# Kernel optimization log

Measured on AMD Instinct MI355X. Metric: run time of the kernel, lower is better.

The kernel has to match this reference:

```python
import jax, jax.numpy as jnp
import numpy as np

B, T, DEMO = 64, 4096, 8
N_MOD, N_POS = 37, 10
D_IN = N_POS + 1 + N_MOD  # 48
PHI_W, LATENT = 128, 128
PSI_W, PSI_L = 128, 128
DOT, HEADS = 64, 4
RHO_W, OUT = 128, 1
MAX_TIME = 1000.0


def _dense_init(key, fan_in, fan_out):
    lim = float(np.sqrt(6.0 / fan_in))  # he_uniform-ish
    return jax.random.uniform(key, (fan_in, fan_out), jnp.float32, -lim, lim)


def setup_inputs() -> dict:
    key = jax.random.key(0)
    ks = jax.random.split(key, 32)
    inp = {}
    inp['demo'] = jax.random.normal(ks[0], (B, DEMO), jnp.float32)
    inp['times'] = jax.random.uniform(ks[1], (B, T, 1), jnp.float32, 0.0, 100.0)
    inp['values'] = jax.random.normal(ks[2], (B, T, 1), jnp.float32)
    inp['measurements'] = jax.random.randint(ks[3], (B, T), 0, N_MOD, jnp.int32)
    # all sequences full length -> N = B*(T+1) static
    inp['segment_ids'] = jnp.repeat(jnp.arange(B, dtype=jnp.int32), T + 1)
    inp['timescales'] = jnp.asarray(MAX_TIME ** np.linspace(0.0, 1.0, N_POS // 2), jnp.float32)
    inp['demo_W1'] = _dense_init(ks[4], DEMO, PHI_W); inp['demo_b1'] = jnp.zeros((PHI_W,), jnp.float32)
    inp['demo_W2'] = _dense_init(ks[5], PHI_W, D_IN); inp['demo_b2'] = jnp.zeros((D_IN,), jnp.float32)
    dims = [D_IN, PHI_W, PHI_W, PHI_W, LATENT]
    for i in range(4):
        inp['phi_W%d' % i] = _dense_init(ks[6 + i], dims[i], dims[i + 1])
        inp['phi_b%d' % i] = jnp.zeros((dims[i + 1],), jnp.float32)
    pdims = [D_IN, PSI_W, PSI_W, PSI_L]
    for i in range(3):
        inp['psi_W%d' % i] = _dense_init(ks[10 + i], pdims[i], pdims[i + 1])
        inp['psi_b%d' % i] = jnp.zeros((pdims[i + 1],), jnp.float32)
    inp['W_k'] = _dense_init(ks[13], PSI_L + D_IN, DOT * HEADS)
    # original inits W_q to zeros (degenerate uniform attention); small random keeps test non-trivial
    inp['W_q'] = jax.random.normal(ks[14], (HEADS, DOT), jnp.float32) * 0.05
    rdims = [LATENT * HEADS, RHO_W, RHO_W, RHO_W, OUT]
    for i in range(4):
        inp['rho_W%d' % i] = _dense_init(ks[15 + i], rdims[i], rdims[i + 1])
        inp['rho_b%d' % i] = jnp.zeros((rdims[i + 1],), jnp.float32)
    return inp


def _forward(demo, times, values, timescales,
             demo_W1, demo_b1, demo_W2, demo_b2,
             phi_W0, phi_b0, phi_W1, phi_b1, phi_W2, phi_b2, phi_W3, phi_b3,
             psi_W0, psi_b0, psi_W1, psi_b1, psi_W2, psi_b2,
             W_k, W_q,
             rho_W0, rho_b0, rho_W1, rho_b1, rho_W2, rho_b2, rho_W3, rho_b3,
             measurements, segment_ids):
    relu = jax.nn.relu
    nseg = demo.shape[0]
    # positional encoding: times [B,T,1] / timescales [5] -> sin|cos -> [B,T,10]
    scaled = times / timescales[None, None, :]
    tt = jnp.concatenate([jnp.sin(scaled), jnp.cos(scaled)], axis=-1)
    meas = jax.nn.one_hot(measurements, N_MOD, dtype=times.dtype)  # [B,T,37]
    combined = jnp.concatenate([tt, values, meas], axis=-1)        # [B,T,48]
    demo_enc = relu(demo @ demo_W1 + demo_b1) @ demo_W2 + demo_b2  # [B,48]
    x = jnp.concatenate([demo_enc[:, None, :], combined], axis=1)  # [B,T+1,48]
    collected = x.reshape(-1, x.shape[-1])                         # [N,48]
    # phi MLP -> encoded [N,LATENT]
    h = collected
    for W, b in ((phi_W0, phi_b0), (phi_W1, phi_b1), (phi_W2, phi_b2), (phi_W3, phi_b3)):
        h = relu(h @ W + b)
    encoded = h
    # psi MLP -> [N,PSI_L], then per-segment mean, scattered back
    p = collected
    for W, b in ((psi_W0, psi_b0), (psi_W1, psi_b1), (psi_W2, psi_b2)):
        p = relu(p @ W + b)
    seg_sum = jax.ops.segment_sum(p, segment_ids, num_segments=nseg)
    counts = jax.ops.segment_sum(jnp.ones((p.shape[0],), p.dtype), segment_ids, num_segments=nseg)
    agg = seg_sum / counts[:, None]
    comb2 = jnp.concatenate([collected, agg[segment_ids]], axis=-1)  # [N, 48+128]
    keys = (comb2 @ W_k).reshape(-1, HEADS, DOT)                     # [N,H,D]
    preattn = jnp.einsum('nhd,hd->nh', keys, W_q) / jnp.sqrt(jnp.float32(DOT))
    # segment softmax per head
    m = jax.ops.segment_max(preattn, segment_ids, num_segments=nseg)
    e = jnp.exp(preattn - m[segment_ids])
    s = jax.ops.segment_sum(e, segment_ids, num_segments=nseg)
    attn = e / s[segment_ids]                                        # [N,H]
    # head-major weighted concat: [N, H*LATENT]
    weighted = (attn[:, :, None] * encoded[:, None, :]).reshape(-1, HEADS * LATENT)
    agg_out = jax.ops.segment_sum(weighted, segment_ids, num_segments=nseg)  # [B,512]
    r = agg_out
    for W, b in ((rho_W0, rho_b0), (rho_W1, rho_b1), (rho_W2, rho_b2)):
        r = relu(r @ W + b)
    return jax.nn.sigmoid(r @ rho_W3 + rho_b3)  # [B,1]


def reference(demo, times, values, timescales,
              demo_W1, demo_b1, demo_W2, demo_b2,
              phi_W0, phi_b0, phi_W1, phi_b1, phi_W2, phi_b2, phi_W3, phi_b3,
              psi_W0, psi_b0, psi_W1, psi_b1, psi_W2, psi_b2,
              W_k, W_q,
              rho_W0, rho_b0, rho_W1, rho_b1, rho_W2, rho_b2, rho_W3, rho_b3,
              measurements, segment_ids):
    return _forward(demo, times, values, timescales,
                    demo_W1, demo_b1, demo_W2, demo_b2,
                    phi_W0, phi_b0, phi_W1, phi_b1, phi_W2, phi_b2, phi_W3, phi_b3,
                    psi_W0, psi_b0, psi_W1, psi_b1, psi_W2, psi_b2,
                    W_k, W_q,
                    rho_W0, rho_b0, rho_W1, rho_b1, rho_W2, rho_b2, rho_W3, rho_b3,
                    measurements, segment_ids)
```

## Files before the change

kernel.cpp:

```cpp
#include <hip/hip_runtime.h>
#include <hip/hip_bf16.h>
#include <math.h>


#define BSEG 64
#define TLEN 4096
#define NPART 17
#define PART_STRIDE 520

#define OFF_DEMO 0
#define OFF_WQ   3072
#define OFF_WT   3264
#define OFF_PARTIALS 31936

typedef __attribute__((ext_vector_type(8))) short short8;
typedef __attribute__((ext_vector_type(4))) float f32x4;
typedef __attribute__((ext_vector_type(2))) float f32x2;

static __device__ __forceinline__ float bfbits2f(unsigned v) { return __uint_as_float(v << 16); }
static __device__ __forceinline__ unsigned short f2bf_rne(float x) {
  unsigned u = __float_as_uint(x);
  unsigned r = (u + 0x7FFFu + ((u >> 16) & 1u)) >> 16;
  return (unsigned short)r;
}
static __device__ __forceinline__ unsigned pk2(float a, float b) {
  float2 f2 = make_float2(a, b);
  __hip_bfloat162 h = __float22bfloat162_rn(f2);
  unsigned u;
  __builtin_memcpy(&u, &h, 4);
  return u;
}

__global__ __launch_bounds__(256) void k_prep(
    const float* __restrict__ demo, const float* __restrict__ dW1, const float* __restrict__ db1,
    const float* __restrict__ dW2, const float* __restrict__ db2,
    const float* __restrict__ Wk, const float* __restrict__ Wq,
    const float* __restrict__ W0, const float* __restrict__ W1,
    const float* __restrict__ W2, const float* __restrict__ W3,
    float* __restrict__ ws) {
  __shared__ float drow[8];
  __shared__ float hdrow[128];
  int bid = blockIdx.x, tid = threadIdx.x;
  if (bid < 224) {
    unsigned short* wt = (unsigned short*)(ws + OFF_WT);
    int i = bid * 256 + tid;
    float v;
    if (i < 8192) {
      int n = i >> 6, k = i & 63;
      v = (k < 48) ? W0[k * 128 + n] : 0.f;
    } else {
      int j = i - 8192;
      int l = j >> 14, r = j & 16383;
      int n = r >> 7, k = r & 127;
      const float* W = (l == 0) ? W1 : (l == 1) ? W2 : W3;
      v = W[k * 128 + n];
    }
    wt[i] = f2bf_rne(v);
    return;
  }
  if (bid == 224) {
    if (tid < 192) {
      int i = tid >> 2, h = tid & 3;
      float a = 0.f;
      for (int d = 0; d < 64; ++d) a = fmaf(Wk[i * 256 + h * 64 + d], Wq[h * 64 + d], a);
      ws[OFF_WQ + tid] = a * 0.125f;
    }
    return;
  }
  int r = bid - 225;
  if (tid < 8) drow[tid] = demo[r * 8 + tid];
  __syncthreads();
  if (tid < 128) {
    float a = db1[tid];
#pragma unroll
    for (int i = 0; i < 8; ++i) a = fmaf(drow[i], dW1[i * 128 + tid], a);
    hdrow[tid] = fmaxf(a, 0.f);
  }
  __syncthreads();
  if (tid < 48) {
    float a = db2[tid];
    for (int k = 0; k < 128; ++k) a = fmaf(hdrow[k], dW2[k * 48 + tid], a);
    ws[OFF_DEMO + r * 48 + tid] = a;
  }
}

template<int MT>
static __device__ __forceinline__ void mfma_layer_T(
    const unsigned short* hin, unsigned short* hout,
    const short8 (&Wf)[2][4], const f32x4 (&bias4)[2],
    int l16, int quad, int n0) {
  const f32x4 z4 = {0.f, 0.f, 0.f, 0.f};
#pragma unroll
  for (int mt = 0; mt < MT; ++mt) {
    short8 Bv[4];
#pragma unroll
    for (int s = 0; s < 4; ++s)
      Bv[s] = *(const short8*)(hin + (mt * 16 + l16) * 136 + s * 32 + quad * 8);
    f32x4 a0 = bias4[0], a1 = bias4[1];
    __builtin_amdgcn_s_setprio(1);
#pragma unroll
    for (int s = 0; s < 4; ++s) {
      a0 = __builtin_amdgcn_mfma_f32_16x16x32_bf16(Wf[0][s], Bv[s], a0, 0, 0, 0);
      a1 = __builtin_amdgcn_mfma_f32_16x16x32_bf16(Wf[1][s], Bv[s], a1, 0, 0, 0);
    }
    __builtin_amdgcn_s_setprio(0);
    f32x4 r0 = __builtin_elementwise_max(a0, z4);
    f32x4 r1 = __builtin_elementwise_max(a1, z4);
    uint4 o;
    o.x = pk2(r0[0], r0[1]);
    o.y = pk2(r0[2], r0[3]);
    o.z = pk2(r1[0], r1[1]);
    o.w = pk2(r1[2], r1[3]);
    *(uint4*)(hout + (mt * 16 + l16) * 136 + n0 + quad * 8) = o;
  }
}
template<int MT>
static __device__ __forceinline__ void mfma_layer0_T(
    const unsigned short* cin, unsigned short* hout,
    const short8 (&Wf)[2][2], const f32x4 (&bias4)[2],
    int l16, int quad, int n0) {
  const f32x4 z4 = {0.f, 0.f, 0.f, 0.f};
#pragma unroll
  for (int mt = 0; mt < MT; ++mt) {
    short8 Bv[2];
#pragma unroll
    for (int s = 0; s < 2; ++s)
      Bv[s] = *(const short8*)(cin + (mt * 16 + l16) * 72 + s * 32 + quad * 8);
    f32x4 a0 = bias4[0], a1 = bias4[1];
    __builtin_amdgcn_s_setprio(1);
    a0 = __builtin_amdgcn_mfma_f32_16x16x32_bf16(Wf[0][0], Bv[0], a0, 0, 0, 0);
    a0 = __builtin_amdgcn_mfma_f32_16x16x32_bf16(Wf[0][1], Bv[1], a0, 0, 0, 0);
    a1 = __builtin_amdgcn_mfma_f32_16x16x32_bf16(Wf[1][0], Bv[0], a1, 0, 0, 0);
    a1 = __builtin_amdgcn_mfma_f32_16x16x32_bf16(Wf[1][1], Bv[1], a1, 0, 0, 0);
    __builtin_amdgcn_s_setprio(0);
    f32x4 r0 = __builtin_elementwise_max(a0, z4);
    f32x4 r1 = __builtin_elementwise_max(a1, z4);
    uint4 o;
    o.x = pk2(r0[0], r0[1]);
    o.y = pk2(r0[2], r0[3]);
    o.z = pk2(r1[0], r1[1]);
    o.w = pk2(r1[2], r1[3]);
    *(uint4*)(hout + (mt * 16 + l16) * 136 + n0 + quad * 8) = o;
  }
}

__global__ __launch_bounds__(256, 2) void k_main(
    const float* __restrict__ times, const float* __restrict__ values,
    const int* __restrict__ meas, const float* __restrict__ tsc,
    const float* __restrict__ ws,
    const float* __restrict__ b0g, const float* __restrict__ b1g,
    const float* __restrict__ b2g, const float* __restrict__ b3g,
    float* __restrict__ part) {
  __shared__ __align__(16) unsigned short hA[64 * 136];
  __shared__ __align__(16) unsigned short hB[64 * 136];
  __shared__ __align__(16) float preb[256 * 4];
  __shared__ __align__(16) float wql[192];
  __shared__ float mred[16];
  int tid = threadIdx.x;
  const int lane = tid & 63, wv = tid >> 6, quad = lane >> 4, l16 = lane & 15;
  const int n0 = wv * 32;

  const int b = blockIdx.x >> 4, c = blockIdx.x & 15;
  const int t0 = c << 8;
  float tv = 0.f, vvv = 0.f;
  int mm = 0;
  float invts[5];
  if (blockIdx.x < 1024) {
    int t = t0 + tid;
    tv = times[b * TLEN + t];
    vvv = values[b * TLEN + t];
    mm = meas[b * TLEN + t];
#pragma unroll
    for (int i = 0; i < 5; ++i) invts[i] = 1.f / tsc[i];
  }

  const unsigned short* wt = (const unsigned short*)(ws + OFF_WT);
  short8 B0[2][2], B1[2][4], B2[2][4], B3[2][4];
  f32x4 bias0[2], bias1[2], bias2[2];
  float bias3[2];
#pragma unroll
  for (int t = 0; t < 2; ++t) {
    int n  = n0 + ((l16 >> 2) << 3) + t * 4 + (l16 & 3);
    int nq = n0 + quad * 8 + t * 4;
    bias0[t] = *(const f32x4*)(b0g + nq);
    bias1[t] = *(const f32x4*)(b1g + nq);
    bias2[t] = *(const f32x4*)(b2g + nq);
    bias3[t] = b3g[n];
#pragma unroll
    for (int s = 0; s < 2; ++s)
      B0[t][s] = *(const short8*)(wt + n * 64 + s * 32 + quad * 8);
#pragma unroll
    for (int s = 0; s < 4; ++s) {
      B1[t][s] = *(const short8*)(wt + 8192  + n * 128 + s * 32 + quad * 8);
      B2[t][s] = *(const short8*)(wt + 24576 + n * 128 + s * 32 + quad * 8);
      B3[t][s] = *(const short8*)(wt + 40960 + n * 128 + s * 32 + quad * 8);
    }
  }
  if (tid < 192) wql[tid] = ws[OFF_WQ + tid];
  __syncthreads();

  if (blockIdx.x == 1024) {
    {
      int r = tid >> 2, cs = tid & 3;
      unsigned short seg[16];
#pragma unroll
      for (int i = 0; i < 16; ++i) seg[i] = 0;
      if (cs < 3)
#pragma unroll
        for (int i = 0; i < 16; ++i) seg[i] = f2bf_rne(ws[OFF_DEMO + r * 48 + cs * 16 + i]);
      unsigned u[8];
#pragma unroll
      for (int i = 0; i < 8; ++i) u[i] = (unsigned)seg[2 * i] | ((unsigned)seg[2 * i + 1] << 16);
      uint4* dst = (uint4*)(hB + r * 72 + cs * 16);
      dst[0] = make_uint4(u[0], u[1], u[2], u[3]);
      dst[1] = make_uint4(u[4], u[5], u[6], u[7]);
    }
    {
      int r = tid >> 2, h = tid & 3;
      float a = 0.f;
      for (int i = 0; i < 48; ++i) a = fmaf(ws[OFF_DEMO + r * 48 + i], wql[i * 4 + h], a);
      preb[tid] = __expf(a);
    }
    f32x4 bias34[2];
#pragma unroll
    for (int t = 0; t < 2; ++t) bias34[t] = *(const f32x4*)(b3g + n0 + quad * 8 + t * 4);
    __syncthreads();
    mfma_layer0_T<4>(hB, hA, B0, bias0, l16, quad, n0); __syncthreads();
    mfma_layer_T<4>(hA, hB, B1, bias1, l16, quad, n0); __syncthreads();
    mfma_layer_T<4>(hB, hA, B2, bias2, l16, quad, n0); __syncthreads();
    mfma_layer_T<4>(hA, hB, B3, bias34, l16, quad, n0); __syncthreads();
    {
      int r = tid >> 2, h = tid & 3;
      part[(r * NPART + 16) * PART_STRIDE + 4 + h] = preb[tid];
    }
    for (int i = tid; i < 64 * 512; i += 256) {
      int r = i >> 9, rem = i & 511;
      int h = rem >> 7, l = rem & 127;
      part[(r * NPART + 16) * PART_STRIDE + 8 + rem] =
          preb[r * 4 + h] * bfbits2f(hB[r * 136 + l]);
    }
    return;
  }

  float s4[4];
  unsigned usv[8];
  const f32x4* wql4 = (const f32x4*)wql;
  {
    float f[11];
#pragma unroll
    for (int i = 0; i < 5; ++i) { float s = tv * invts[i]; f[i] = __sinf(s); f[5 + i] = __cosf(s); }
    f[10] = vvv;
    f32x4 a4 = wql4[11 + mm];
#pragma unroll
    for (int i = 0; i < 11; ++i) {
      f32x4 fi = {f[i], f[i], f[i], f[i]};
      a4 = __builtin_elementwise_fma(fi, wql4[i], a4);
    }
    float e0 = __expf(a4[0]), e1 = __expf(a4[1]);
    float e2 = __expf(a4[2]), e3 = __expf(a4[3]);
    *(f32x4*)(preb + tid * 4) = (f32x4){e0, e1, e2, e3};
    s4[0] = e0; s4[1] = e1; s4[2] = e2; s4[3] = e3;
    int kk = 11 + mm;
    usv[0] = pk2(f[0], f[1]); usv[1] = pk2(f[2], f[3]);
    usv[2] = pk2(f[4], f[5]); usv[3] = pk2(f[6], f[7]);
    usv[4] = pk2(f[8], f[9]);
    usv[5] = pk2(f[10], (kk == 11) ? 1.f : 0.f);
    usv[6] = ((kk == 12) ? 0x3F80u : 0u) | ((kk == 13) ? 0x3F800000u : 0u);
    usv[7] = ((kk == 14) ? 0x3F80u : 0u) | ((kk == 15) ? 0x3F800000u : 0u);
  }

  auto build_tile = [&](int tile) {
    int r = lane;
    if (wv == tile) {
      uint4* dst = (uint4*)(hB + r * 72);
      dst[0] = make_uint4(usv[0], usv[1], usv[2], usv[3]);
      dst[1] = make_uint4(usv[4], usv[5], usv[6], usv[7]);
      uint4 z = make_uint4(0u, 0u, 0u, 0u);
      *(uint4*)(hB + r * 72 + 48) = z;
      *(uint4*)(hB + r * 72 + 56) = z;
    } else if (wv == (tile ^ 1)) {
      int t = t0 + tile * 64 + r;
      int mmf = meas[b * TLEN + t];
      int kk = 11 + mmf;
      uint4 z = make_uint4(0u, 0u, 0u, 0u);
      uint4* dst = (uint4*)(hB + r * 72 + 16);
#pragma unroll
      for (int k = 0; k < 4; ++k) dst[k] = z;
      asm volatile("" ::: "memory");
      if (kk >= 16) hB[r * 72 + kk] = 0x3F80;
    }
  };

  f32x2 pacc2[2][2] = {{{0.f, 0.f}, {0.f, 0.f}}, {{0.f, 0.f}, {0.f, 0.f}}};
  const f32x4 z4 = {0.f, 0.f, 0.f, 0.f};
  const int ncb = n0 + ((l16 >> 2) << 3) + (l16 & 3);
  build_tile(0);
  for (int tile = 0; tile < 4; ++tile) {
    int rb = tile << 6;
    __syncthreads();
    mfma_layer0_T<4>(hB, hA, B0, bias0, l16, quad, n0); __syncthreads();
    mfma_layer_T<4>(hA, hB, B1, bias1, l16, quad, n0); __syncthreads();
    mfma_layer_T<4>(hB, hA, B2, bias2, l16, quad, n0); __syncthreads();
    if (tile < 3) build_tile(tile + 1);
#pragma unroll
    for (int mt = 0; mt < 4; ++mt) {
      short8 A[4];
#pragma unroll
      for (int s = 0; s < 4; ++s)
        A[s] = *(const short8*)(hA + (mt * 16 + l16) * 136 + s * 32 + quad * 8);
      f32x4 acc0 = {bias3[0], bias3[0], bias3[0], bias3[0]};
      f32x4 acc1 = {bias3[1], bias3[1], bias3[1], bias3[1]};
      __builtin_amdgcn_s_setprio(1);
#pragma unroll
      for (int s = 0; s < 4; ++s) {
        acc0 = __builtin_amdgcn_mfma_f32_16x16x32_bf16(A[s], B3[0][s], acc0, 0, 0, 0);
        acc1 = __builtin_amdgcn_mfma_f32_16x16x32_bf16(A[s], B3[1][s], acc1, 0, 0, 0);
      }
      __builtin_amdgcn_s_setprio(0);
      f32x4 r0 = __builtin_elementwise_max(acc0, z4);
      f32x4 r1 = __builtin_elementwise_max(acc1, z4);
#pragma unroll
      for (int j = 0; j < 4; ++j) {
        int row = rb + mt * 16 + quad * 4 + j;
        f32x4 e4 = *(const f32x4*)(preb + row * 4);
        f32x2 e01 = {e4[0], e4[1]}, e23 = {e4[2], e4[3]};
        f32x2 v0 = {r0[j], r0[j]}, v1 = {r1[j], r1[j]};
        pacc2[0][0] = __builtin_elementwise_fma(v0, e01, pacc2[0][0]);
        pacc2[0][1] = __builtin_elementwise_fma(v0, e23, pacc2[0][1]);
        pacc2[1][0] = __builtin_elementwise_fma(v1, e01, pacc2[1][0]);
        pacc2[1][1] = __builtin_elementwise_fma(v1, e23, pacc2[1][1]);
      }
    }
  }
  float pacc[2][4];
#pragma unroll
  for (int t = 0; t < 2; ++t)
#pragma unroll
    for (int h = 0; h < 4; ++h) pacc[t][h] = pacc2[t][h >> 1][h & 1];
#pragma unroll
  for (int t = 0; t < 2; ++t)
#pragma unroll
    for (int h = 0; h < 4; ++h) {
      float v = pacc[t][h];
      v += __shfl_xor(v, 16, 64);
      v += __shfl_xor(v, 32, 64);
      pacc[t][h] = v;
    }
#pragma unroll
  for (int off = 32; off > 0; off >>= 1)
#pragma unroll
    for (int h = 0; h < 4; ++h) s4[h] += __shfl_xor(s4[h], off, 64);
  if (lane == 0)
#pragma unroll
    for (int h = 0; h < 4; ++h) mred[wv * 4 + h] = s4[h];
  __syncthreads();
  float* P = part + (b * NPART + c) * PART_STRIDE;
  if (tid < 4) P[4 + tid] = mred[tid] + mred[4 + tid] + mred[8 + tid] + mred[12 + tid];
  if (quad == 0)
#pragma unroll
    for (int t = 0; t < 2; ++t)
#pragma unroll
      for (int h = 0; h < 4; ++h)
        P[8 + h * 128 + (ncb + t * 4)] = pacc[t][h];
}

__global__ __launch_bounds__(256) void k_combine(
    const float* __restrict__ part,
    const float* __restrict__ rW0, const float* __restrict__ rb0,
    const float* __restrict__ rW1, const float* __restrict__ rb1,
    const float* __restrict__ rW2, const float* __restrict__ rb2,
    const float* __restrict__ rW3, const float* __restrict__ rb3,
    float* __restrict__ out) {
  __shared__ float Ss[4], agg[512], r1[128], p0[256];
  int tid = threadIdx.x;
  int b = blockIdx.x;
  const float* P = part + b * NPART * PART_STRIDE;
  if (tid < 4) {
    float s = 0.f;
    for (int p = 0; p < NPART; ++p) s += P[p * PART_STRIDE + 4 + tid];
    Ss[tid] = s;
  }
  __syncthreads();
  for (int idx = tid; idx < 512; idx += 256) {
    int h = idx >> 7;
    float a = 0.f;
    for (int p = 0; p < NPART; ++p) a += P[p * PART_STRIDE + 8 + idx];
    agg[idx] = a / Ss[h];
  }
  __syncthreads();
  const int col = tid & 127, half = tid >> 7;
  {
    float a = 0.f;
    for (int k = half * 256; k < half * 256 + 256; ++k) a = fmaf(agg[k], rW0[k * 128 + col], a);
    p0[tid] = a;
  }
  __syncthreads();
  if (tid < 128) r1[tid] = fmaxf(rb0[tid] + p0[tid] + p0[128 + tid], 0.f);
  __syncthreads();
  {
    float a = 0.f;
    for (int k = half * 64; k < half * 64 + 64; ++k) a = fmaf(r1[k], rW1[k * 128 + col], a);
    p0[tid] = a;
  }
  __syncthreads();
  if (tid < 128) r1[tid] = fmaxf(rb1[tid] + p0[tid] + p0[128 + tid], 0.f);
  __syncthreads();
  {
    float a = 0.f;
    for (int k = half * 64; k < half * 64 + 64; ++k) a = fmaf(r1[k], rW2[k * 128 + col], a);
    p0[tid] = a;
  }
  __syncthreads();
  if (tid < 128) p0[tid] = fmaxf(rb2[tid] + p0[tid] + p0[128 + tid], 0.f) * rW3[tid];
  __syncthreads();
  if (tid < 64) {
    float v = p0[tid] + p0[tid + 64];
#pragma unroll
    for (int off = 32; off > 0; off >>= 1) v += __shfl_xor(v, off, 64);
    if (tid == 0) out[b] = 1.f / (1.f + __expf(-(rb3[0] + v)));
  }
}

extern "C" void kernel_launch(void* const* d_in, const int* in_sizes, int n_in,
                              void* d_out, int out_size, void* d_ws, size_t ws_size,
                              hipStream_t stream) {
  const float* demo   = (const float*)d_in[0];
  const float* times  = (const float*)d_in[1];
  const float* values = (const float*)d_in[2];
  const int*   meas   = (const int*)d_in[3];
  const float* tsc = (const float*)d_in[5];
  const float* dW1 = (const float*)d_in[6];
  const float* db1 = (const float*)d_in[7];
  const float* dW2 = (const float*)d_in[8];
  const float* db2 = (const float*)d_in[9];
  const float* pW0 = (const float*)d_in[10];
  const float* pb0 = (const float*)d_in[11];
  const float* pW1 = (const float*)d_in[12];
  const float* pb1 = (const float*)d_in[13];
  const float* pW2 = (const float*)d_in[14];
  const float* pb2 = (const float*)d_in[15];
  const float* pW3 = (const float*)d_in[16];
  const float* pb3 = (const float*)d_in[17];
  const float* Wk  = (const float*)d_in[24];
  const float* Wq  = (const float*)d_in[25];
  const float* rW0 = (const float*)d_in[26];
  const float* rb0 = (const float*)d_in[27];
  const float* rW1 = (const float*)d_in[28];
  const float* rb1 = (const float*)d_in[29];
  const float* rW2 = (const float*)d_in[30];
  const float* rb2 = (const float*)d_in[31];
  const float* rW3 = (const float*)d_in[32];
  const float* rb3 = (const float*)d_in[33];
  float* ws = (float*)d_ws;
  float* partials = ws + OFF_PARTIALS;

  k_prep<<<289, 256, 0, stream>>>(demo, dW1, db1, dW2, db2, Wk, Wq,
                                  pW0, pW1, pW2, pW3, ws);
  k_main<<<1025, 256, 0, stream>>>(times, values, meas, tsc, ws,
                                   pb0, pb1, pb2, pb3, partials);
  k_combine<<<64, 256, 0, stream>>>(partials, rW0, rb0, rW1, rb1, rW2, rb2, rW3, rb3,
                                    (float*)d_out);
}
```

Before: 191.7 us.

## Double block size to 512 threads, splitting rows across two wave groups

The main kernel now runs 512-thread blocks that each cover 512 timesteps. Eight waves split into two row groups of 64 rows that share the same output-column slices, so the block count and the partial buffers per sequence are halved. The aim is to spread the per-block cost of loading MFMA weights into registers over twice as many rows and to cut the partial-sum traffic read by the combine kernel. In exchange, LDS use per block roughly doubles and a cross-group reduction through shared memory is added, which may lower occupancy. The build_tile zeroing work is also moved to a third thread group.

```diff
diff --git a/kernel.cpp b/kernel.cpp
--- a/kernel.cpp
+++ b/kernel.cpp
@@ -5,7 +5,7 @@
 
 #define BSEG 64
 #define TLEN 4096
-#define NPART 17
+#define NPART 9
 #define PART_STRIDE 520
 
 #define OFF_DEMO 0
@@ -88,14 +88,14 @@
 static __device__ __forceinline__ void mfma_layer_T(
     const unsigned short* hin, unsigned short* hout,
     const short8 (&Wf)[2][4], const f32x4 (&bias4)[2],
-    int l16, int quad, int n0) {
+    int l16, int quad, int n0, int ro) {
   const f32x4 z4 = {0.f, 0.f, 0.f, 0.f};
 #pragma unroll
   for (int mt = 0; mt < MT; ++mt) {
     short8 Bv[4];
 #pragma unroll
     for (int s = 0; s < 4; ++s)
-      Bv[s] = *(const short8*)(hin + (mt * 16 + l16) * 136 + s * 32 + quad * 8);
+      Bv[s] = *(const short8*)(hin + (ro + mt * 16 + l16) * 136 + s * 32 + quad * 8);
     f32x4 a0 = bias4[0], a1 = bias4[1];
     __builtin_amdgcn_s_setprio(1);
 #pragma unroll
@@ -111,21 +111,21 @@
     o.y = pk2(r0[2], r0[3]);
     o.z = pk2(r1[0], r1[1]);
     o.w = pk2(r1[2], r1[3]);
-    *(uint4*)(hout + (mt * 16 + l16) * 136 + n0 + quad * 8) = o;
+    *(uint4*)(hout + (ro + mt * 16 + l16) * 136 + n0 + quad * 8) = o;
   }
 }
 template<int MT>
 static __device__ __forceinline__ void mfma_layer0_T(
     const unsigned short* cin, unsigned short* hout,
     const short8 (&Wf)[2][2], const f32x4 (&bias4)[2],
-    int l16, int quad, int n0) {
+    int l16, int quad, int n0, int ro) {
   const f32x4 z4 = {0.f, 0.f, 0.f, 0.f};
 #pragma unroll
   for (int mt = 0; mt < MT; ++mt) {
     short8 Bv[2];
 #pragma unroll
     for (int s = 0; s < 2; ++s)
-      Bv[s] = *(const short8*)(cin + (mt * 16 + l16) * 72 + s * 32 + quad * 8);
+      Bv[s] = *(const short8*)(cin + (ro + mt * 16 + l16) * 72 + s * 32 + quad * 8);
     f32x4 a0 = bias4[0], a1 = bias4[1];
     __builtin_amdgcn_s_setprio(1);
     a0 = __builtin_amdgcn_mfma_f32_16x16x32_bf16(Wf[0][0], Bv[0], a0, 0, 0, 0);
@@ -140,32 +140,35 @@
     o.y = pk2(r0[2], r0[3]);
     o.z = pk2(r1[0], r1[1]);
     o.w = pk2(r1[2], r1[3]);
-    *(uint4*)(hout + (mt * 16 + l16) * 136 + n0 + quad * 8) = o;
-  }
-}
-
-__global__ __launch_bounds__(256, 2) void k_main(
+    *(uint4*)(hout + (ro + mt * 16 + l16) * 136 + n0 + quad * 8) = o;
+  }
+}
+
+__global__ __launch_bounds__(512, 2) void k_main(
     const float* __restrict__ times, const float* __restrict__ values,
     const int* __restrict__ meas, const float* __restrict__ tsc,
     const float* __restrict__ ws,
     const float* __restrict__ b0g, const float* __restrict__ b1g,
     const float* __restrict__ b2g, const float* __restrict__ b3g,
     float* __restrict__ part) {
-  __shared__ __align__(16) unsigned short hA[64 * 136];
-  __shared__ __align__(16) unsigned short hB[64 * 136];
-  __shared__ __align__(16) float preb[256 * 4];
+  __shared__ __align__(16) unsigned short hA[128 * 136];
+  __shared__ __align__(16) unsigned short hB[128 * 136];
+  __shared__ __align__(16) float preb[512 * 4];
   __shared__ __align__(16) float wql[192];
-  __shared__ float mred[16];
+  __shared__ float mred[32];
   int tid = threadIdx.x;
   const int lane = tid & 63, wv = tid >> 6, quad = lane >> 4, l16 = lane & 15;
-  const int n0 = wv * 32;
-
-  const int b = blockIdx.x >> 4, c = blockIdx.x & 15;
-  const int t0 = c << 8;
+  const int wf = wv & 3;
+  const int wr = wv >> 2;
+  const int n0 = wf * 32;
+  const int ro = wr * 64;
+
+  const int b = blockIdx.x >> 3, c = blockIdx.x & 7;
+  const int t0 = c << 9;
   float tv = 0.f, vvv = 0.f;
   int mm = 0;
   float invts[5];
-  if (blockIdx.x < 1024) {
+  if (blockIdx.x < 512) {
     int t = t0 + tid;
     tv = times[b * TLEN + t];
     vvv = values[b * TLEN + t];
@@ -199,8 +202,8 @@
   if (tid < 192) wql[tid] = ws[OFF_WQ + tid];
   __syncthreads();
 
-  if (blockIdx.x == 1024) {
-    {
+  if (blockIdx.x == 512) {
+    if (tid < 256) {
       int r = tid >> 2, cs = tid & 3;
       unsigned short seg[16];
 #pragma unroll
@@ -215,7 +218,7 @@
       dst[0] = make_uint4(u[0], u[1], u[2], u[3]);
       dst[1] = make_uint4(u[4], u[5], u[6], u[7]);
     }
-    {
+    if (tid < 256) {
       int r = tid >> 2, h = tid & 3;
       float a = 0.f;
       for (int i = 0; i < 48; ++i) a = fmaf(ws[OFF_DEMO + r * 48 + i], wql[i * 4 + h], a);
@@ -224,19 +227,20 @@
     f32x4 bias34[2];
 #pragma unroll
     for (int t = 0; t < 2; ++t) bias34[t] = *(const f32x4*)(b3g + n0 + quad * 8 + t * 4);
+    const int rd = wr * 32;
     __syncthreads();
-    mfma_layer0_T<4>(hB, hA, B0, bias0, l16, quad, n0); __syncthreads();
-    mfma_layer_T<4>(hA, hB, B1, bias1, l16, quad, n0); __syncthreads();
-    mfma_layer_T<4>(hB, hA, B2, bias2, l16, quad, n0); __syncthreads();
-    mfma_layer_T<4>(hA, hB, B3, bias34, l16, quad, n0); __syncthreads();
-    {
+    mfma_layer0_T<2>(hB, hA, B0, bias0, l16, quad, n0, rd); __syncthreads();
+    mfma_layer_T<2>(hA, hB, B1, bias1, l16, quad, n0, rd); __syncthreads();
+    mfma_layer_T<2>(hB, hA, B2, bias2, l16, quad, n0, rd); __syncthreads();
+    mfma_layer_T<2>(hA, hB, B3, bias34, l16, quad, n0, rd); __syncthreads();
+    if (tid < 256) {
       int r = tid >> 2, h = tid & 3;
-      part[(r * NPART + 16) * PART_STRIDE + 4 + h] = preb[tid];
-    }
-    for (int i = tid; i < 64 * 512; i += 256) {
+      part[(r * NPART + 8) * PART_STRIDE + 4 + h] = preb[tid];
+    }
+    for (int i = tid; i < 64 * 512; i += 512) {
       int r = i >> 9, rem = i & 511;
       int h = rem >> 7, l = rem & 127;
-      part[(r * NPART + 16) * PART_STRIDE + 8 + rem] =
+      part[(r * NPART + 8) * PART_STRIDE + 8 + rem] =
           preb[r * 4 + h] * bfbits2f(hB[r * 136 + l]);
     }
     return;
@@ -270,16 +274,13 @@
   }
 
   auto build_tile = [&](int tile) {
-    int r = lane;
-    if (wv == tile) {
+    int q = tid >> 7, r = tid & 127;
+    if (q == tile) {
       uint4* dst = (uint4*)(hB + r * 72);
       dst[0] = make_uint4(usv[0], usv[1], usv[2], usv[3]);
       dst[1] = make_uint4(usv[4], usv[5], usv[6], usv[7]);
-      uint4 z = make_uint4(0u, 0u, 0u, 0u);
-      *(uint4*)(hB + r * 72 + 48) = z;
-      *(uint4*)(hB + r * 72 + 56) = z;
-    } else if (wv == (tile ^ 1)) {
-      int t = t0 + tile * 64 + r;
+    } else if (q == (tile ^ 1)) {
+      int t = t0 + tile * 128 + r;
       int mmf = meas[b * TLEN + t];
       int kk = 11 + mmf;
       uint4 z = make_uint4(0u, 0u, 0u, 0u);
@@ -288,6 +289,10 @@
       for (int k = 0; k < 4; ++k) dst[k] = z;
       asm volatile("" ::: "memory");
       if (kk >= 16) hB[r * 72 + kk] = 0x3F80;
+    } else if (q == (tile ^ 2)) {
+      uint4 z = make_uint4(0u, 0u, 0u, 0u);
+      *(uint4*)(hB + r * 72 + 48) = z;
+      *(uint4*)(hB + r * 72 + 56) = z;
     }
   };
 
@@ -296,18 +301,18 @@
   const int ncb = n0 + ((l16 >> 2) << 3) + (l16 & 3);
   build_tile(0);
   for (int tile = 0; tile < 4; ++tile) {
-    int rb = tile << 6;
+    int rb = tile << 7;
     __syncthreads();
-    mfma_layer0_T<4>(hB, hA, B0, bias0, l16, quad, n0); __syncthreads();
-    mfma_layer_T<4>(hA, hB, B1, bias1, l16, quad, n0); __syncthreads();
-    mfma_layer_T<4>(hB, hA, B2, bias2, l16, quad, n0); __syncthreads();
+    mfma_layer0_T<4>(hB, hA, B0, bias0, l16, quad, n0, ro); __syncthreads();
+    mfma_layer_T<4>(hA, hB, B1, bias1, l16, quad, n0, ro); __syncthreads();
+    mfma_layer_T<4>(hB, hA, B2, bias2, l16, quad, n0, ro); __syncthreads();
     if (tile < 3) build_tile(tile + 1);
 #pragma unroll
     for (int mt = 0; mt < 4; ++mt) {
       short8 A[4];
 #pragma unroll
       for (int s = 0; s < 4; ++s)
-        A[s] = *(const short8*)(hA + (mt * 16 + l16) * 136 + s * 32 + quad * 8);
+        A[s] = *(const short8*)(hA + (ro + mt * 16 + l16) * 136 + s * 32 + quad * 8);
       f32x4 acc0 = {bias3[0], bias3[0], bias3[0], bias3[0]};
       f32x4 acc1 = {bias3[1], bias3[1], bias3[1], bias3[1]};
       __builtin_amdgcn_s_setprio(1);
@@ -321,7 +326,7 @@
       f32x4 r1 = __builtin_elementwise_max(acc1, z4);
 #pragma unroll
       for (int j = 0; j < 4; ++j) {
-        int row = rb + mt * 16 + quad * 4 + j;
+        int row = rb + ro + mt * 16 + quad * 4 + j;
         f32x4 e4 = *(const f32x4*)(preb + row * 4);
         f32x2 e01 = {e4[0], e4[1]}, e23 = {e4[2], e4[3]};
         f32x2 v0 = {r0[j], r0[j]}, v1 = {r1[j], r1[j]};
@@ -354,14 +359,28 @@
 #pragma unroll
     for (int h = 0; h < 4; ++h) mred[wv * 4 + h] = s4[h];
   __syncthreads();
+  float* pbuf = preb;
+  if (wr == 1 && quad == 0)
+#pragma unroll
+    for (int t = 0; t < 2; ++t)
+#pragma unroll
+      for (int h = 0; h < 4; ++h)
+        pbuf[wf * 128 + t * 64 + h * 16 + l16] = pacc[t][h];
+  __syncthreads();
   float* P = part + (b * NPART + c) * PART_STRIDE;
-  if (tid < 4) P[4 + tid] = mred[tid] + mred[4 + tid] + mred[8 + tid] + mred[12 + tid];
-  if (quad == 0)
+  if (tid < 4) {
+    float s = 0.f;
+#pragma unroll
+    for (int w = 0; w < 8; ++w) s += mred[w * 4 + tid];
+    P[4 + tid] = s;
+  }
+  if (wr == 0 && quad == 0)
 #pragma unroll
     for (int t = 0; t < 2; ++t)
 #pragma unroll
       for (int h = 0; h < 4; ++h)
-        P[8 + h * 128 + (ncb + t * 4)] = pacc[t][h];
+        P[8 + h * 128 + (ncb + t * 4)] =
+            pacc[t][h] + pbuf[wf * 128 + t * 64 + h * 16 + l16];
 }
 
 __global__ __launch_bounds__(256) void k_combine(
@@ -456,8 +475,8 @@
 
   k_prep<<<289, 256, 0, stream>>>(demo, dW1, db1, dW2, db2, Wk, Wq,
                                   pW0, pW1, pW2, pW3, ws);
-  k_main<<<1025, 256, 0, stream>>>(times, values, meas, tsc, ws,
-                                   pb0, pb1, pb2, pb3, partials);
+  k_main<<<513, 512, 0, stream>>>(times, values, meas, tsc, ws,
+                                  pb0, pb1, pb2, pb3, partials);
   k_combine<<<64, 256, 0, stream>>>(partials, rW0, rb0, rW1, rb1, rW2, rb2, rW3, rb3,
                                     (float*)d_out);
 }
```

New measurement: 197.3 us. 1.03x slower.
